# Performance work log

Hardware: AMD Instinct MI355X
Metric: run time of the kernel (lower is better)

## Reference

```python
import jax, jax.numpy as jnp
import numpy as np

H = 2048        # hidden_dim
D = 128         # head_dim
NQ = H // D     # 16 query heads
NKV = 4         # kv heads (GQA)
ROTARY_BASE = 10000.0


def _rope_cos_sin(seq_len, dim, dtype):
    inv_freq = 1.0 / (ROTARY_BASE ** (jnp.arange(0, dim, 2, dtype=jnp.float32) / dim))
    t = jnp.arange(seq_len, dtype=jnp.float32)
    freqs = jnp.outer(t, inv_freq)          # [S, D/2]
    return jnp.cos(freqs).astype(dtype), jnp.sin(freqs).astype(dtype)


def _apply_rope(x, cos, sin):
    # x: [B, S, H, D], non-interleaved (rotate-half) convention of flash-attn
    d2 = x.shape[-1] // 2
    x1, x2 = x[..., :d2], x[..., d2:]
    c = cos[None, :, None, :]
    s = sin[None, :, None, :]
    return jnp.concatenate([x1 * c - x2 * s, x2 * c + x1 * s], axis=-1)


def setup_inputs() -> dict:
    key = jax.random.key(0)
    ks = jax.random.split(key, 9)
    B, S = 2, 2048
    sd = 1.0 / np.sqrt(H)
    return {
        "hidden_states": jax.random.normal(ks[0], (B, S, H), jnp.float32),
        "Wq": jax.random.normal(ks[1], (H, NQ * D), jnp.float32) * sd,
        "bq": jnp.zeros((NQ * D,), jnp.float32),
        "Wk": jax.random.normal(ks[2], (H, NKV * D), jnp.float32) * sd,
        "bk": jnp.zeros((NKV * D,), jnp.float32),
        "Wv": jax.random.normal(ks[3], (H, NKV * D), jnp.float32) * sd,
        "bv": jnp.zeros((NKV * D,), jnp.float32),
        "Wc": jax.random.normal(ks[4], (NQ * D, H), jnp.float32) * sd,
        "bc": jnp.zeros((H,), jnp.float32),
    }


def reference(hidden_states, Wq, bq, Wk, bk, Wv, bv, Wc, bc):
    B, S, _ = hidden_states.shape
    scale = 1.0 / np.sqrt(D)  # scale_attn_by_inverse_layer_idx=False

    q = (hidden_states @ Wq + bq).reshape(B, S, NQ, D)
    k = (hidden_states @ Wk + bk).reshape(B, S, NKV, D)
    v = (hidden_states @ Wv + bv).reshape(B, S, NKV, D)

    cos, sin = _rope_cos_sin(S, D, q.dtype)
    q = _apply_rope(q, cos, sin)
    k = _apply_rope(k, cos, sin)

    # GQA: expand kv heads to match query heads
    rep = NQ // NKV
    k_e = jnp.repeat(k, rep, axis=2)  # [B, S, NQ, D]
    v_e = jnp.repeat(v, rep, axis=2)

    scores = jnp.einsum("bshd,bthd->bhst", q, k_e) * scale  # [B, NQ, S, S]
    causal = jnp.tril(jnp.ones((S, S), bool))
    scores = jnp.where(causal[None, None], scores, jnp.finfo(scores.dtype).min)
    probs = jax.nn.softmax(scores, axis=-1)
    attn = jnp.einsum("bhst,bthd->bshd", probs, v_e)  # [B, S, NQ, D]

    out = attn.reshape(B, S, NQ * D) @ Wc + bc  # resid dropout p=0 (eval)
    return out, k, v
```

## Files before the change

### kernel.cpp

```cpp
#include <hip/hip_runtime.h>
#include <math.h>

typedef unsigned short u16;
typedef __attribute__((ext_vector_type(8))) short s16x8;
typedef __attribute__((ext_vector_type(4))) float f32x4;
typedef __attribute__((ext_vector_type(16))) float f32x16;

#define B_  2
#define S_  2048
#define H_  2048
#define D_  128
#define NQ_ 16
#define NKV_ 4
#define M_  (B_*S_)
#define NQKV_ 3072

#define MFMA16(a,b,c) __builtin_amdgcn_mfma_f32_16x16x32_bf16(a,b,c,0,0,0)
#define MFMA32(a,b,c) __builtin_amdgcn_mfma_f32_32x32x16_bf16(a,b,c,0,0,0)

__device__ __forceinline__ u16 f2bf(float x) {
  union { float f; unsigned u; } v; v.f = x;
  unsigned r = v.u + 0x7fffu + ((v.u >> 16) & 1u);
  return (u16)(r >> 16);
}

__device__ __forceinline__ unsigned cvtpk(float lo, float hi) {
  unsigned r;
  asm("v_cvt_pk_bf16_f32 %0, %1, %2" : "=v"(r) : "v"(lo), "v"(hi));
  return r;
}

__global__ __launch_bounds__(256) void cvt_x(const float* __restrict__ X, u16* __restrict__ Xb, long n4) {
  const f32x4* X4 = (const f32x4*)X;
  for (long i = (long)blockIdx.x*256 + threadIdx.x; i < n4; i += (long)gridDim.x*256) {
    f32x4 v = X4[i];
    union { u16 u[4]; unsigned long long ll; } p;
    p.u[0] = f2bf(v[0]); p.u[1] = f2bf(v[1]); p.u[2] = f2bf(v[2]); p.u[3] = f2bf(v[3]);
    ((unsigned long long*)Xb)[i] = p.ll;
  }
}

__global__ __launch_bounds__(256) void wtrans(const float* __restrict__ W, u16* __restrict__ Wt,
                                              int N, int K) {
  __shared__ float t[32][33];
  const int n0 = blockIdx.x*32, k0 = blockIdx.y*32;
  const int tx = threadIdx.x, ty = threadIdx.y;
  #pragma unroll
  for (int i = 0; i < 32; i += 8) t[ty+i][tx] = W[(long)(k0+ty+i)*N + n0 + tx];
  __syncthreads();
  #pragma unroll
  for (int i = 0; i < 32; i += 8) Wt[(long)(n0+ty+i)*K + k0 + tx] = f2bf(t[tx][ty+i]);
}

__global__ __launch_bounds__(256) void vtrans(const float* __restrict__ QKV, u16* __restrict__ Vt) {
  __shared__ float t[32][33];
  const int bk = blockIdx.z;
  const int s0 = blockIdx.x*32, d0 = blockIdx.y*32;
  const int tx = threadIdx.x, ty = threadIdx.y;
  const int b = bk >> 2, kvh = bk & 3;
  #pragma unroll
  for (int i = 0; i < 32; i += 8)
    t[ty+i][tx] = QKV[(long)(b*S_ + s0+ty+i)*NQKV_ + 2560 + kvh*128 + d0 + tx];
  __syncthreads();
  #pragma unroll
  for (int i = 0; i < 32; i += 8)
    Vt[((long)bk*D_ + d0+ty+i)*S_ + s0 + tx] = f2bf(t[tx][ty+i]);
}

__global__ void concat_bias(const float* bq, const float* bk, const float* bv, float* bqkv) {
  int i = blockIdx.x*256 + threadIdx.x;
  if (i < NQKV_)
    bqkv[i] = (i < 2048) ? bq[i] : ((i < 2560) ? bk[i-2048] : bv[i-2560]);
}

__global__ void rope_tab(float* __restrict__ cosb, float* __restrict__ sinb) {
  int i = blockIdx.x*256 + threadIdx.x;
  int t = i >> 6, d = i & 63;
  float inv = powf(10000.0f, -((float)(2*d)) * (1.0f/128.0f));
  float fr = (float)t * inv;
  float sv, cv;
  sincosf(fr, &sv, &cv);
  cosb[i] = cv; sinb[i] = sv;
}

__global__ __launch_bounds__(256) void rope_qkv(
    const float* __restrict__ QKV, const float* __restrict__ cosb, const float* __restrict__ sinb,
    u16* __restrict__ Qb, u16* __restrict__ Kb,
    float* __restrict__ kout, float* __restrict__ vout)
{
  const float QS = 0.08838834764831845f * 1.4426950408889634f;
  const int m = blockIdx.x;
  const int b = m >> 11, s = m & 2047;
  const int tid = threadIdx.x;
  const float* row = QKV + (long)m * NQKV_;
  const int d = tid & 63;
  const float c  = cosb[s*64 + d];
  const float sn = sinb[s*64 + d];
  #pragma unroll
  for (int i = 0; i < 4; i++) {
    int hh = (tid + i*256) >> 6;
    float x1 = row[hh*128 + d], x2 = row[hh*128 + d + 64];
    float o1 = x1*c - x2*sn, o2 = x2*c + x1*sn;
    long base = ((long)(b*NQ_ + hh)*S_ + s)*D_;
    Qb[base + d] = f2bf(o1*QS);
    Qb[base + d + 64] = f2bf(o2*QS);
  }
  {
    int kh = tid >> 6;
    float x1 = row[2048 + kh*128 + d], x2 = row[2048 + kh*128 + d + 64];
    float o1 = x1*c - x2*sn, o2 = x2*c + x1*sn;
    long kb = ((long)(b*NKV_ + kh)*S_ + s)*D_;
    Kb[kb + d] = f2bf(o1);
    Kb[kb + d + 64] = f2bf(o2);
    long ko = ((long)m*NKV_ + kh)*D_;
    kout[ko + d] = o1;
    kout[ko + d + 64] = o2;
  }
  #pragma unroll
  for (int i = 0; i < 2; i++) {
    int e = tid + i*256;
    vout[(long)m*512 + e] = row[2560 + e];
  }
}

__global__ __launch_bounds__(256) void gemm_bt(
    const u16* __restrict__ A, const u16* __restrict__ B,
    const float* __restrict__ bias, float* __restrict__ C,
    int M, int N, int K)
{
  __shared__ u16 As[128*32];
  __shared__ u16 Bs[128*32];
  const int tid = threadIdx.x;
  const int lane = tid & 63, w = tid >> 6;
  const int r16 = lane & 15, g = lane >> 4;
  const int gx = gridDim.x;
  const int nwg = gx * gridDim.y;
  const int id = blockIdx.y * gx + blockIdx.x;
  const int cpx = nwg >> 3;
  const int sid = (id & 7) * cpx + (id >> 3);
  const long m0 = (long)(sid / gx) * 128;
  const long n0 = (long)(sid % gx) * 128;
  const int wr = w >> 1, wc = w & 1;
  f32x4 acc[4][4] = {};

  const u16* Ag = A + m0 * K;
  const u16* Bg = B + n0 * K;

  for (int k0 = 0; k0 < K; k0 += 32) {
    #pragma unroll
    for (int it = 0; it < 2; it++) {
      int c = it*256 + w*64 + lane;
      const u16* ga = Ag + (long)(c >> 2) * K + k0 + (c & 3) * 8;
      __builtin_amdgcn_global_load_lds(
          (const __attribute__((address_space(1))) unsigned int*)ga,
          (__attribute__((address_space(3))) unsigned int*)&As[(it*256 + w*64)*8], 16, 0, 0);
      const u16* gb = Bg + (long)(c >> 2) * K + k0 + (c & 3) * 8;
      __builtin_amdgcn_global_load_lds(
          (const __attribute__((address_space(1))) unsigned int*)gb,
          (__attribute__((address_space(3))) unsigned int*)&Bs[(it*256 + w*64)*8], 16, 0, 0);
    }
    __syncthreads();
    s16x8 af[4], bf[4];
    #pragma unroll
    for (int mi = 0; mi < 4; mi++)
      af[mi] = *(const s16x8*)&As[(wr*64 + mi*16 + r16)*32 + g*8];
    #pragma unroll
    for (int nj = 0; nj < 4; nj++)
      bf[nj] = *(const s16x8*)&Bs[(wc*64 + nj*16 + r16)*32 + g*8];
    #pragma unroll
    for (int mi = 0; mi < 4; mi++)
      #pragma unroll
      for (int nj = 0; nj < 4; nj++)
        acc[mi][nj] = MFMA16(af[mi], bf[nj], acc[mi][nj]);
    __syncthreads();
  }

  #pragma unroll
  for (int mi = 0; mi < 4; mi++) {
    #pragma unroll
    for (int nj = 0; nj < 4; nj++) {
      int col = wc*64 + nj*16 + r16;
      float bv = bias[n0 + col];
      #pragma unroll
      for (int r = 0; r < 4; r++) {
        int row = wr*64 + mi*16 + g*4 + r;
        C[(m0 + row) * N + n0 + col] = acc[mi][nj][r] + bv;
      }
    }
  }
}

__global__ __launch_bounds__(256, 2) void attn_kernel(
    const u16* __restrict__ Qb, const u16* __restrict__ Kb,
    const u16* __restrict__ Vt, u16* __restrict__ Ob)
{
  __shared__ u16 Ks[2][64*128];
  __shared__ u16 Vs[2][128*64];
  const int tid = threadIdx.x;
  const int lane = tid & 63, w = tid >> 6;
  const int l31 = lane & 31, hi = lane >> 5;
  const int id = blockIdx.x;
  const int bh = id & 31;
  const int b = bh >> 4, h = bh & 15;
  const int p = id >> 5;
  const int qt = (p < 8) ? p : (23 - p);
  const int kvh = h >> 2;
  const int q0w = qt*128 + w*32;
  const int nt = 2*qt + 2;

  const u16* Qg = Qb + (((long)(b*NQ_ + h))*S_ + q0w)*D_;
  const u16* Kg = Kb + ((long)(b*NKV_ + kvh))*S_*D_;
  const u16* Vg = Vt + ((long)(b*NKV_ + kvh))*D_*S_;

  s16x8 qf[8];
  #pragma unroll
  for (int ks = 0; ks < 8; ks++)
    qf[ks] = *(const s16x8*)&Qg[l31*D_ + ks*16 + hi*8];

  f32x16 po[4] = {};
  float mrow = -1e30f, lrow = 0.f;

  auto stage = [&](int buf, int kv0s) {
    #pragma unroll
    for (int i = 0; i < 4; i++) {
      const int c = i*4 + w;
      const int G = c*64 + lane;
      const int krow = G >> 4, kcg = G & 15;
      const u16* gk = Kg + (long)(kv0s + krow)*D_ + ((kcg ^ (krow & 15)) * 8);
      __builtin_amdgcn_global_load_lds(
          (const __attribute__((address_space(1))) unsigned int*)gk,
          (__attribute__((address_space(3))) unsigned int*)&Ks[buf][c*512], 16, 0, 0);
      const int vrow = G >> 3, vcg = G & 7;
      const u16* gv = Vg + (long)vrow*S_ + kv0s + ((vcg ^ (vrow & 7)) * 8);
      __builtin_amdgcn_global_load_lds(
          (const __attribute__((address_space(1))) unsigned int*)gv,
          (__attribute__((address_space(3))) unsigned int*)&Vs[buf][c*512], 16, 0, 0);
    }
  };

  stage(0, 0);
  for (int t = 0; t < nt; t++) {
    const int cur = t & 1;
    const int kv0 = t*64;
    if (t + 1 < nt) {
      stage(cur ^ 1, kv0 + 64);
      asm volatile("s_waitcnt vmcnt(8)" ::: "memory");
    } else {
      asm volatile("s_waitcnt vmcnt(0)" ::: "memory");
    }
    __builtin_amdgcn_s_barrier();

    if (kv0 <= q0w + 31) {
      f32x16 sc[2] = {};
      #pragma unroll
      for (int ks = 0; ks < 8; ks++) {
        #pragma unroll
        for (int ct = 0; ct < 2; ct++) {
          const int row = ct*32 + l31;
          s16x8 kf = *(const s16x8*)&Ks[cur][row*128 + ((ks*16 + hi*8) ^ ((row & 15)*8))];
          sc[ct] = MFMA32(kf, qf[ks], sc[ct]);
        }
      }
      if (kv0 + 63 > q0w) {
        const int qrow = q0w + l31;
        #pragma unroll
        for (int ct = 0; ct < 2; ct++)
          #pragma unroll
          for (int r = 0; r < 16; r++) {
            int kv = kv0 + ct*32 + (r & 3) + 8*(r >> 2) + 4*hi;
            if (kv > qrow) sc[ct][r] = -3.0e38f;
          }
      }
      float pm = sc[0][0];
      #pragma unroll
      for (int ct = 0; ct < 2; ct++)
        #pragma unroll
        for (int r = 0; r < 16; r++) pm = fmaxf(pm, sc[ct][r]);
      pm = fmaxf(pm, __shfl_xor(pm, 32, 64));
      if (!__all(pm - mrow <= 8.0f)) {
        float mn = fmaxf(mrow, pm);
        float fr = exp2f(mrow - mn);
        mrow = mn;
        lrow *= fr;
        #pragma unroll
        for (int r = 0; r < 16; r++) {
          float frv = __shfl(fr, (r & 3) + 8*(r >> 2) + 4*hi, 64);
          #pragma unroll
          for (int dt = 0; dt < 4; dt++) po[dt][r] *= frv;
        }
      }
      float ps = 0.f;
      #pragma unroll
      for (int ct = 0; ct < 2; ct++)
        #pragma unroll
        for (int r = 0; r < 16; r++) {
          float pv = exp2f(sc[ct][r] - mrow);
          sc[ct][r] = pv;
          ps += pv;
        }
      ps += __shfl_xor(ps, 32, 64);
      lrow += ps;
      unsigned mw[2][8], ex[2][8];
      #pragma unroll
      for (int ct = 0; ct < 2; ct++)
        #pragma unroll
        for (int wd = 0; wd < 8; wd++)
          mw[ct][wd] = cvtpk(sc[ct][2*wd], sc[ct][2*wd + 1]);
      #pragma unroll
      for (int ct = 0; ct < 2; ct++)
        #pragma unroll
        for (int wd = 0; wd < 8; wd++)
          ex[ct][wd] = __shfl_xor((int)mw[ct][wd], 32, 64);
      s16x8 pa[4];
      #pragma unroll
      for (int ct = 0; ct < 2; ct++)
        #pragma unroll
        for (int pp = 0; pp < 2; pp++) {
          union { unsigned u[4]; s16x8 v; } pu;
          pu.u[0] = hi ? ex[ct][4*pp + 2] : mw[ct][4*pp + 0];
          pu.u[1] = hi ? ex[ct][4*pp + 3] : mw[ct][4*pp + 1];
          pu.u[2] = hi ? mw[ct][4*pp + 2] : ex[ct][4*pp + 0];
          pu.u[3] = hi ? mw[ct][4*pp + 3] : ex[ct][4*pp + 1];
          pa[ct*2 + pp] = pu.v;
        }
      #pragma unroll
      for (int ks2 = 0; ks2 < 4; ks2++)
        #pragma unroll
        for (int dt = 0; dt < 4; dt++) {
          const int row = dt*32 + l31;
          s16x8 vf = *(const s16x8*)&Vs[cur][row*64 + ((ks2*16 + hi*8) ^ ((row & 7)*8))];
          po[dt] = MFMA32(pa[ks2], vf, po[dt]);
        }
    }
    __builtin_amdgcn_s_barrier();
  }

  float inv = 1.0f / lrow;
  #pragma unroll
  for (int r = 0; r < 16; r++) {
    const int qr = (r & 3) + 8*(r >> 2) + 4*hi;
    float invq = __shfl(inv, qr, 64);
    const long q = (long)q0w + qr;
    #pragma unroll
    for (int dt = 0; dt < 4; dt++)
      Ob[((long)b*S_ + q)*H_ + h*D_ + dt*32 + l31] = f2bf(po[dt][r]*invq);
  }
}

extern "C" void kernel_launch(void* const* d_in, const int* in_sizes, int n_in,
                              void* d_out, int out_size, void* d_ws, size_t ws_size,
                              hipStream_t stream) {
  const float* hs = (const float*)d_in[0];
  const float* Wq = (const float*)d_in[1];
  const float* bq = (const float*)d_in[2];
  const float* Wk = (const float*)d_in[3];
  const float* bk = (const float*)d_in[4];
  const float* Wv = (const float*)d_in[5];
  const float* bv = (const float*)d_in[6];
  const float* Wc = (const float*)d_in[7];
  const float* bc = (const float*)d_in[8];

  float* out  = (float*)d_out;
  float* kout = out + (long)M_*H_;
  float* vout = kout + (long)M_*NKV_*D_;

  char* ws = (char*)d_ws;
  u16*  Xbf   = (u16*)ws;
  u16*  Wqkvt = Xbf + (long)M_*H_;
  u16*  Wct   = Wqkvt + (long)NQKV_*H_;
  float* bqkv = (float*)(Wct + (long)H_*H_);
  float* QKV  = bqkv + NQKV_;
  float* cosb = QKV + (long)M_*NQKV_;
  float* sinb = cosb + S_*64;
  u16*  Qbf   = (u16*)(sinb + S_*64);
  u16*  Kbf   = Qbf + (long)B_*NQ_*S_*D_;
  u16*  Vtb   = Kbf + (long)B_*NKV_*S_*D_;
  u16*  Obf   = Vtb + (long)B_*NKV_*D_*S_;

  cvt_x<<<2048, 256, 0, stream>>>(hs, Xbf, (long)M_*H_/4);
  wtrans<<<dim3(64,64), dim3(32,8), 0, stream>>>(Wq, Wqkvt, 2048, 2048);
  wtrans<<<dim3(16,64), dim3(32,8), 0, stream>>>(Wk, Wqkvt + 2048L*2048, 512, 2048);
  wtrans<<<dim3(16,64), dim3(32,8), 0, stream>>>(Wv, Wqkvt + 2560L*2048, 512, 2048);
  wtrans<<<dim3(64,64), dim3(32,8), 0, stream>>>(Wc, Wct, 2048, 2048);
  concat_bias<<<12, 256, 0, stream>>>(bq, bk, bv, bqkv);
  rope_tab<<<512, 256, 0, stream>>>(cosb, sinb);

  gemm_bt<<<dim3(NQKV_/128, M_/128), 256, 0, stream>>>(Xbf, Wqkvt, bqkv, QKV, M_, NQKV_, H_);
  rope_qkv<<<M_, 256, 0, stream>>>(QKV, cosb, sinb, Qbf, Kbf, kout, vout);
  vtrans<<<dim3(S_/32, D_/32, B_*NKV_), dim3(32,8), 0, stream>>>(QKV, Vtb);
  attn_kernel<<<dim3(512), 256, 0, stream>>>(Qbf, Kbf, Vtb, Obf);
  gemm_bt<<<dim3(H_/128, M_/128), 256, 0, stream>>>(Obf, Wct, bc, out, M_, H_, H_);
}
```

Measured before the change: 242.8 us.

## Replace GEMMs with double-buffered 256-row swizzled tiles and bf16 QKV intermediate

```diff
diff --git a/kernel.cpp b/kernel.cpp
--- a/kernel.cpp
+++ b/kernel.cpp
@@ -23,6 +23,10 @@
   unsigned r = v.u + 0x7fffu + ((v.u >> 16) & 1u);
   return (u16)(r >> 16);
 }
+__device__ __forceinline__ float bf2f(u16 x) {
+  union { unsigned u; float f; } v; v.u = ((unsigned)x) << 16;
+  return v.f;
+}
 
 __device__ __forceinline__ unsigned cvtpk(float lo, float hi) {
   unsigned r;
@@ -52,8 +56,8 @@
   for (int i = 0; i < 32; i += 8) Wt[(long)(n0+ty+i)*K + k0 + tx] = f2bf(t[tx][ty+i]);
 }
 
-__global__ __launch_bounds__(256) void vtrans(const float* __restrict__ QKV, u16* __restrict__ Vt) {
-  __shared__ float t[32][33];
+__global__ __launch_bounds__(256) void vtrans(const u16* __restrict__ QKV, u16* __restrict__ Vt) {
+  __shared__ u16 t[32][33];
   const int bk = blockIdx.z;
   const int s0 = blockIdx.x*32, d0 = blockIdx.y*32;
   const int tx = threadIdx.x, ty = threadIdx.y;
@@ -64,7 +68,7 @@
   __syncthreads();
   #pragma unroll
   for (int i = 0; i < 32; i += 8)
-    Vt[((long)bk*D_ + d0+ty+i)*S_ + s0 + tx] = f2bf(t[tx][ty+i]);
+    Vt[((long)bk*D_ + d0+ty+i)*S_ + s0 + tx] = t[tx][ty+i];
 }
 
 __global__ void concat_bias(const float* bq, const float* bk, const float* bv, float* bqkv) {
@@ -84,7 +88,7 @@
 }
 
 __global__ __launch_bounds__(256) void rope_qkv(
-    const float* __restrict__ QKV, const float* __restrict__ cosb, const float* __restrict__ sinb,
+    const u16* __restrict__ QKV, const float* __restrict__ cosb, const float* __restrict__ sinb,
     u16* __restrict__ Qb, u16* __restrict__ Kb,
     float* __restrict__ kout, float* __restrict__ vout)
 {
@@ -92,14 +96,14 @@
   const int m = blockIdx.x;
   const int b = m >> 11, s = m & 2047;
   const int tid = threadIdx.x;
-  const float* row = QKV + (long)m * NQKV_;
+  const u16* row = QKV + (long)m * NQKV_;
   const int d = tid & 63;
   const float c  = cosb[s*64 + d];
   const float sn = sinb[s*64 + d];
   #pragma unroll
   for (int i = 0; i < 4; i++) {
     int hh = (tid + i*256) >> 6;
-    float x1 = row[hh*128 + d], x2 = row[hh*128 + d + 64];
+    float x1 = bf2f(row[hh*128 + d]), x2 = bf2f(row[hh*128 + d + 64]);
     float o1 = x1*c - x2*sn, o2 = x2*c + x1*sn;
     long base = ((long)(b*NQ_ + hh)*S_ + s)*D_;
     Qb[base + d] = f2bf(o1*QS);
@@ -107,7 +111,7 @@
   }
   {
     int kh = tid >> 6;
-    float x1 = row[2048 + kh*128 + d], x2 = row[2048 + kh*128 + d + 64];
+    float x1 = bf2f(row[2048 + kh*128 + d]), x2 = bf2f(row[2048 + kh*128 + d + 64]);
     float o1 = x1*c - x2*sn, o2 = x2*c + x1*sn;
     long kb = ((long)(b*NKV_ + kh)*S_ + s)*D_;
     Kb[kb + d] = f2bf(o1);
@@ -119,72 +123,114 @@
   #pragma unroll
   for (int i = 0; i < 2; i++) {
     int e = tid + i*256;
-    vout[(long)m*512 + e] = row[2560 + e];
-  }
-}
-
-__global__ __launch_bounds__(256) void gemm_bt(
-    const u16* __restrict__ A, const u16* __restrict__ B,
-    const float* __restrict__ bias, float* __restrict__ C,
+    vout[(long)m*512 + e] = bf2f(row[2560 + e]);
+  }
+}
+
+template<int BN, typename OutT>
+__global__ __launch_bounds__(512, 2) void gemm256(
+    const u16* __restrict__ A, const u16* __restrict__ Bm,
+    const float* __restrict__ bias, OutT* __restrict__ C,
     int M, int N, int K)
 {
-  __shared__ u16 As[128*32];
-  __shared__ u16 Bs[128*32];
+  __shared__ u16 As[2][256*64];
+  __shared__ u16 Bs[2][BN*64];
+  constexpr int WCc = (BN == 256) ? 4 : 2;
+  constexpr int MI  = (BN == 256) ? 8 : 4;
+  constexpr int LB  = BN/64;
+  constexpr int TOT = 4 + LB;
+
   const int tid = threadIdx.x;
   const int lane = tid & 63, w = tid >> 6;
   const int r16 = lane & 15, g = lane >> 4;
+  const int wrn = w / WCc, wcn = w % WCc;
+  const int abase = wrn * (MI*16);
+  const int bbase = wcn * 64;
+
   const int gx = gridDim.x;
   const int nwg = gx * gridDim.y;
   const int id = blockIdx.y * gx + blockIdx.x;
   const int cpx = nwg >> 3;
   const int sid = (id & 7) * cpx + (id >> 3);
-  const long m0 = (long)(sid / gx) * 128;
-  const long n0 = (long)(sid % gx) * 128;
-  const int wr = w >> 1, wc = w & 1;
-  f32x4 acc[4][4] = {};
+  const long m0 = (long)(sid / gx) * 256;
+  const long n0 = (long)(sid % gx) * BN;
 
   const u16* Ag = A + m0 * K;
-  const u16* Bg = B + n0 * K;
-
-  for (int k0 = 0; k0 < K; k0 += 32) {
-    #pragma unroll
-    for (int it = 0; it < 2; it++) {
-      int c = it*256 + w*64 + lane;
-      const u16* ga = Ag + (long)(c >> 2) * K + k0 + (c & 3) * 8;
+  const u16* Bg = Bm + n0 * K;
+
+  auto stage = [&](int buf, int k0) {
+    #pragma unroll
+    for (int i = 0; i < 4; i++) {
+      const int slot = i*512 + tid;
+      const int row = slot >> 3, cg = slot & 7;
+      const u16* src = Ag + (long)row*K + k0 + ((cg ^ (row & 7)) * 8);
       __builtin_amdgcn_global_load_lds(
-          (const __attribute__((address_space(1))) unsigned int*)ga,
-          (__attribute__((address_space(3))) unsigned int*)&As[(it*256 + w*64)*8], 16, 0, 0);
-      const u16* gb = Bg + (long)(c >> 2) * K + k0 + (c & 3) * 8;
+          (const __attribute__((address_space(1))) unsigned int*)src,
+          (__attribute__((address_space(3))) unsigned int*)&As[buf][slot*8], 16, 0, 0);
+    }
+    #pragma unroll
+    for (int i = 0; i < LB; i++) {
+      const int slot = i*512 + tid;
+      const int row = slot >> 3, cg = slot & 7;
+      const u16* src = Bg + (long)row*K + k0 + ((cg ^ (row & 7)) * 8);
       __builtin_amdgcn_global_load_lds(
-          (const __attribute__((address_space(1))) unsigned int*)gb,
-          (__attribute__((address_space(3))) unsigned int*)&Bs[(it*256 + w*64)*8], 16, 0, 0);
-    }
-    __syncthreads();
-    s16x8 af[4], bf[4];
-    #pragma unroll
-    for (int mi = 0; mi < 4; mi++)
-      af[mi] = *(const s16x8*)&As[(wr*64 + mi*16 + r16)*32 + g*8];
-    #pragma unroll
-    for (int nj = 0; nj < 4; nj++)
-      bf[nj] = *(const s16x8*)&Bs[(wc*64 + nj*16 + r16)*32 + g*8];
-    #pragma unroll
-    for (int mi = 0; mi < 4; mi++)
-      #pragma unroll
-      for (int nj = 0; nj < 4; nj++)
-        acc[mi][nj] = MFMA16(af[mi], bf[nj], acc[mi][nj]);
-    __syncthreads();
-  }
-
-  #pragma unroll
-  for (int mi = 0; mi < 4; mi++) {
+          (const __attribute__((address_space(1))) unsigned int*)src,
+          (__attribute__((address_space(3))) unsigned int*)&Bs[buf][slot*8], 16, 0, 0);
+    }
+  };
+
+  f32x4 acc[MI][4] = {};
+  const int nt = K >> 6;
+
+  stage(0, 0);
+  stage(1, 64);
+  for (int t = 0; t < nt; t++) {
+    if (t + 1 < nt) {
+      if constexpr (TOT == 8) asm volatile("s_waitcnt vmcnt(8)" ::: "memory");
+      else                    asm volatile("s_waitcnt vmcnt(6)" ::: "memory");
+    } else {
+      asm volatile("s_waitcnt vmcnt(0)" ::: "memory");
+    }
+    __builtin_amdgcn_s_barrier();
+
+    const u16* as = &As[t & 1][0];
+    const u16* bs = &Bs[t & 1][0];
+    #pragma unroll
+    for (int k = 0; k < 2; k++) {
+      s16x8 bfr[4];
+      #pragma unroll
+      for (int nj = 0; nj < 4; nj++) {
+        const int R = bbase + nj*16 + r16;
+        bfr[nj] = *(const s16x8*)&bs[R*64 + (((k*4 + g) ^ (R & 7)) * 8)];
+      }
+      __builtin_amdgcn_s_setprio(1);
+      #pragma unroll
+      for (int mi = 0; mi < MI; mi++) {
+        const int R = abase + mi*16 + r16;
+        s16x8 afr = *(const s16x8*)&as[R*64 + (((k*4 + g) ^ (R & 7)) * 8)];
+        #pragma unroll
+        for (int nj = 0; nj < 4; nj++)
+          acc[mi][nj] = MFMA16(afr, bfr[nj], acc[mi][nj]);
+      }
+      __builtin_amdgcn_s_setprio(0);
+    }
+    __builtin_amdgcn_s_barrier();
+    if (t + 2 < nt) stage(t & 1, (t + 2) << 6);
+  }
+
+  #pragma unroll
+  for (int mi = 0; mi < MI; mi++) {
     #pragma unroll
     for (int nj = 0; nj < 4; nj++) {
-      int col = wc*64 + nj*16 + r16;
-      float bv = bias[n0 + col];
+      const int col = bbase + nj*16 + r16;
+      const float bv = bias[n0 + col];
       #pragma unroll
       for (int r = 0; r < 4; r++) {
-        int row = wr*64 + mi*16 + g*4 + r;
-        C[(m0 + row) * N + n0 + col] = acc[mi][nj][r] + bv;
+        const long row = m0 + abase + mi*16 + g*4 + r;
+        if constexpr (sizeof(OutT) == 2)
+          C[row * N + n0 + col] = (OutT)f2bf(acc[mi][nj][r] + bv);
+        else
+          C[row * N + n0 + col] = (OutT)(acc[mi][nj][r] + bv);
       }
     }
   }
@@ -369,8 +415,8 @@
   u16*  Wqkvt = Xbf + (long)M_*H_;
   u16*  Wct   = Wqkvt + (long)NQKV_*H_;
   float* bqkv = (float*)(Wct + (long)H_*H_);
-  float* QKV  = bqkv + NQKV_;
-  float* cosb = QKV + (long)M_*NQKV_;
+  u16*  QKV   = (u16*)(bqkv + NQKV_);
+  float* cosb = (float*)(QKV + (long)M_*NQKV_);
   float* sinb = cosb + S_*64;
   u16*  Qbf   = (u16*)(sinb + S_*64);
   u16*  Kbf   = Qbf + (long)B_*NQ_*S_*D_;
@@ -385,9 +431,11 @@
   concat_bias<<<12, 256, 0, stream>>>(bq, bk, bv, bqkv);
   rope_tab<<<512, 256, 0, stream>>>(cosb, sinb);
 
-  gemm_bt<<<dim3(NQKV_/128, M_/128), 256, 0, stream>>>(Xbf, Wqkvt, bqkv, QKV, M_, NQKV_, H_);
+  gemm256<256, u16><<<dim3(NQKV_/256, M_/256), 512, 0, stream>>>(
+      Xbf, Wqkvt, bqkv, QKV, M_, NQKV_, H_);
   rope_qkv<<<M_, 256, 0, stream>>>(QKV, cosb, sinb, Qbf, Kbf, kout, vout);
   vtrans<<<dim3(S_/32, D_/32, B_*NKV_), dim3(32,8), 0, stream>>>(QKV, Vtb);
   attn_kernel<<<dim3(512), 256, 0, stream>>>(Qbf, Kbf, Vtb, Obf);
-  gemm_bt<<<dim3(H_/128, M_/128), 256, 0, stream>>>(Obf, Wct, bc, out, M_, H_, H_);
-}
+  gemm256<128, float><<<dim3(H_/128, M_/256), 512, 0, stream>>>(
+      Obf, Wct, bc, out, M_, H_, H_);
+}
```

Result: faster. 229.3 us (-5.5%).
